# Optimization experiments

Measured on AMD Instinct MI355X. Metric: run time of the kernel, lower is better.

Reference implementation:

```python
import jax, jax.numpy as jnp
import numpy as np

P = 64
K = 64
D = 2048
KERNEL_MUL = 2.0
KERNEL_NUM = 5


def setup_inputs() -> dict:
    key = jax.random.key(0)
    k1, k2 = jax.random.split(key)
    source = jax.random.normal(k1, (P * K, D), dtype=jnp.float32)
    target = jax.random.normal(k2, (P * K, D), dtype=jnp.float32)
    return {"source": source, "target": target}


def _mmd_terms(source, target):
    # split into P groups of K rows each, process all splits at once
    src = source.reshape(P, K, D)
    tgt = target.reshape(P, K, D)
    total = jnp.concatenate([src, tgt], axis=1)          # [P, 2K, D]
    n = 2 * K
    # pairwise squared L2 distances per split: [P, 2K, 2K]
    sq = jnp.sum(total * total, axis=-1)                  # [P, 2K]
    gram = jnp.einsum('pid,pjd->pij', total, total)       # [P, 2K, 2K]
    l2 = sq[:, :, None] + sq[:, None, :] - 2.0 * gram
    # bandwidth from detached distances (torch uses L2_distance.data)
    bw = jax.lax.stop_gradient(jnp.sum(l2, axis=(1, 2))) / (n * n - n)  # [P]
    bw = bw / (KERNEL_MUL ** (KERNEL_NUM // 2))
    mults = KERNEL_MUL ** jnp.arange(KERNEL_NUM, dtype=jnp.float32)     # [kn]
    bws = bw[:, None] * mults[None, :] + 1e-9                           # [P, kn]
    # multi-bandwidth Gaussian kernel sum: [P, 2K, 2K]
    kern = jnp.sum(jnp.exp(-l2[:, None, :, :] / bws[:, :, None, None]), axis=1)
    XX = kern[:, :K, :K]
    YY = kern[:, K:, K:]
    XY = kern[:, :K, K:]
    YX = kern[:, K:, :K]
    xx = jnp.mean(XX, axis=(1, 2))
    yy = jnp.mean(YY, axis=(1, 2))
    xy = jnp.mean(XY, axis=(1, 2))
    yx = jnp.mean(YX, axis=(1, 2))
    per_split_loss = xx + yy - xy - yx                    # [P]
    total_loss = jnp.sum(per_split_loss) / P
    return total_loss, l2, xx, yy, xy, yx


def reference(source, target):
    total_loss, l2, xx, yy, xy, yx = _mmd_terms(source, target)
    # original returns max of l2dist from the LAST split only
    max_l2_last = jnp.max(l2[-1])
    return (total_loss.reshape(1), max_l2_last,
            jnp.sum(xx) / P, jnp.sum(yy) / P, jnp.sum(xy) / P, jnp.sum(yx) / P)
```

## Files before the change

kernel.cpp:

```cpp
#include <hip/hip_runtime.h>

typedef _Float16 half8 __attribute__((ext_vector_type(8)));
typedef _Float16 half4v __attribute__((ext_vector_type(4)));
typedef float floatx4 __attribute__((ext_vector_type(4)));
typedef unsigned int uint2v __attribute__((ext_vector_type(2)));

#define NSPLIT 64
#define KS 64
#define DIM 2048
#define NROW 128
#define BK 128
#define KSPL 4
#define KCH (DIM / KSPL)
#define NKC_A (KCH / BK)
#define SST 152
#define GSZ (NROW * NROW)
#define NBLK (NSPLIT * KSPL)
#define GT2F_OFF (NBLK * GSZ / 2)
#define PART_OFF (GT2F_OFF + NBLK)
#define CNT_OFF (PART_OFF + NBLK * 4)


__device__ __forceinline__ unsigned int pk16(float a, float b) {
  return __builtin_bit_cast(unsigned int, __builtin_amdgcn_cvt_pkrtz(a, b));
}

__global__ __launch_bounds__(1024) void gram_kernel(const float* __restrict__ src,
                                                    const float* __restrict__ tgt,
                                                    float* __restrict__ ws) {
  __shared__ __align__(16) _Float16 stage[2][NROW * SST];
  __shared__ float red[16];

  if (blockIdx.x == 0 && threadIdx.x == 0) *(unsigned*)(ws + CNT_OFF) = 0u;

  const int p = blockIdx.x >> 2;
  const int c = blockIdx.x & (KSPL - 1);
  const int tid = threadIdx.x;
  const int lane = tid & 63;
  const int wave = tid >> 6;

  const int srow = tid >> 3;
  const int c4 = (tid & 7) * 4;
  const float* rowp = ((srow < KS) ? (src + (size_t)(p * KS + srow) * DIM)
                                   : (tgt + (size_t)(p * KS + (srow - KS)) * DIM)) +
                      c * KCH;

  const int wr = (wave >> 2) * 32;
  const int wc = (wave & 3) * 32;
  const int fr = lane & 15;
  const int fk = (lane >> 4) * 8;

  floatx4 acc00 = {0.f, 0.f, 0.f, 0.f};
  floatx4 acc01 = {0.f, 0.f, 0.f, 0.f};
  floatx4 acc10 = {0.f, 0.f, 0.f, 0.f};
  floatx4 acc11 = {0.f, 0.f, 0.f, 0.f};

  float4 f0, f1, f2, f3;
#define LOADK(kc)                                      \
  do {                                                 \
    const float* gp_ = rowp + (kc) * BK + c4;          \
    f0 = *(const float4*)(gp_);                        \
    f1 = *(const float4*)(gp_ + 32);                   \
    f2 = *(const float4*)(gp_ + 64);                   \
    f3 = *(const float4*)(gp_ + 96);                   \
  } while (0)

  LOADK(0);
#pragma unroll
  for (int kc = 0; kc < NKC_A; ++kc) {
    {
      _Float16* sp = &stage[kc & 1][srow * SST + c4];
      *(uint2v*)(sp)      = (uint2v){pk16(f0.x, f0.y), pk16(f0.z, f0.w)};
      *(uint2v*)(sp + 32) = (uint2v){pk16(f1.x, f1.y), pk16(f1.z, f1.w)};
      *(uint2v*)(sp + 64) = (uint2v){pk16(f2.x, f2.y), pk16(f2.z, f2.w)};
      *(uint2v*)(sp + 96) = (uint2v){pk16(f3.x, f3.y), pk16(f3.z, f3.w)};
    }
    if (kc + 1 < NKC_A) LOADK(kc + 1);
    __syncthreads();
    const _Float16* sbuf = stage[kc & 1];
#pragma unroll
    for (int ks = 0; ks < 4; ++ks) {
      const int ko = ks * 32 + fk;
      half8 a0 = *(const half8*)&sbuf[(wr + fr) * SST + ko];
      half8 a1 = *(const half8*)&sbuf[(wr + 16 + fr) * SST + ko];
      half8 b0 = *(const half8*)&sbuf[(wc + fr) * SST + ko];
      half8 b1 = *(const half8*)&sbuf[(wc + 16 + fr) * SST + ko];
      acc00 = __builtin_amdgcn_mfma_f32_16x16x32_f16(a0, b0, acc00, 0, 0, 0);
      acc01 = __builtin_amdgcn_mfma_f32_16x16x32_f16(a0, b1, acc01, 0, 0, 0);
      acc10 = __builtin_amdgcn_mfma_f32_16x16x32_f16(a1, b0, acc10, 0, 0, 0);
      acc11 = __builtin_amdgcn_mfma_f32_16x16x32_f16(a1, b1, acc11, 0, 0, 0);
    }
  }
#undef LOADK

  _Float16* hs = (_Float16*)ws + (size_t)blockIdx.x * GSZ + wave * 1024 + lane * 4;
  {
    half4v h0, h1, h2, h3;
#pragma unroll
    for (int r = 0; r < 4; ++r) {
      h0[r] = (_Float16)acc00[r];
      h1[r] = (_Float16)acc01[r];
      h2[r] = (_Float16)acc10[r];
      h3[r] = (_Float16)acc11[r];
    }
    *(half4v*)(hs)       = h0;
    *(half4v*)(hs + 256) = h1;
    *(half4v*)(hs + 512) = h2;
    *(half4v*)(hs + 768) = h3;
  }

  float gsum = 0.0f;
#pragma unroll
  for (int r = 0; r < 4; ++r) gsum += acc00[r] + acc01[r] + acc10[r] + acc11[r];
#pragma unroll
  for (int m = 1; m <= 32; m <<= 1) gsum += __shfl_xor(gsum, m, 64);
  if (lane == 0) red[wave] = gsum;
  __syncthreads();
  if (tid == 0) {
    float t = 0.0f;
    for (int w = 0; w < 16; ++w) t += red[w];
    ws[GT2F_OFF + blockIdx.x] = t;
  }
}

__global__ __launch_bounds__(1024) void reduce_kernel(float* __restrict__ ws,
                                                      float* __restrict__ out) {
  __shared__ float sqv[NROW];
  __shared__ float bcast[8];
  __shared__ float redm[16];
  __shared__ float redq[16];
  __shared__ float fr2[16][5];
  __shared__ unsigned amLast;

  const int b = blockIdx.x;
  const int p = b >> 2;
  const int rb = b & 3;
  const int tid = threadIdx.x;
  const int lane = tid & 63;
  const int wave = tid >> 6;

  const _Float16* sb = (const _Float16*)ws + (size_t)(p * KSPL) * GSZ;

  const int hoff = rb * 4096 + tid * 4;
  float g0, g1, g2, g3;
  {
    half4v h = *(const half4v*)(sb + hoff);
    g0 = (float)h[0]; g1 = (float)h[1]; g2 = (float)h[2]; g3 = (float)h[3];
#pragma unroll
    for (int c8 = 1; c8 < KSPL; ++c8) {
      half4v hh = *(const half4v*)(sb + (size_t)c8 * GSZ + hoff);
      g0 += (float)hh[0]; g1 += (float)hh[1]; g2 += (float)hh[2]; g3 += (float)hh[3];
    }
  }

  if (tid < NROW) {
    const int i = tid;
    const int wd = (i >> 5) * 5;
    const int ad = ((i >> 4) & 1) * 3;
    const int lnd = (((i & 15) >> 2) << 4) + (i & 15);
    const int idxd = wd * 1024 + ad * 256 + lnd * 4 + (i & 3);
    float d = 0.0f;
#pragma unroll
    for (int c8 = 0; c8 < KSPL; ++c8) d += (float)sb[(size_t)c8 * GSZ + idxd];
    sqv[i] = d;
  }
  __syncthreads();

  if (tid == 0) {
    float ssq = 0.0f;
    for (int i = 0; i < NROW; ++i) ssq += sqv[i];
    float gt = ws[GT2F_OFF + p * 4 + 0] + ws[GT2F_OFF + p * 4 + 1] +
               ws[GT2F_OFF + p * 4 + 2] + ws[GT2F_OFF + p * 4 + 3];
    float suml2 = 2.0f * (float)NROW * ssq - 2.0f * gt;
    float bw = suml2 / (float)(NROW * NROW - NROW) * 0.25f;
    float mult = 1.0f;
    for (int k = 0; k < 5; ++k) {
      bcast[k] = 1.0f / (bw * mult + 1e-9f);
      mult *= 2.0f;
    }
  }
  __syncthreads();

  const int r0 = rb * 32 + ((tid >> 7) & 1) * 16 + ((tid >> 4) & 3) * 4;
  const int col = (tid >> 8) * 32 + ((tid >> 6) & 1) * 16 + (tid & 15);
  const float sqc = sqv[col];
  const floatx4 sr = *(const floatx4*)&sqv[r0];
  const float gg[4] = {g0, g1, g2, g3};
  float l2r[4];
  float lmax = 0.0f;
#pragma unroll
  for (int k = 0; k < 4; ++k) {
    float v = sr[k] + sqc - 2.0f * gg[k];
    l2r[k] = v;
    lmax = fmaxf(lmax, v);
  }
#pragma unroll
  for (int m = 1; m <= 32; m <<= 1) lmax = fmaxf(lmax, __shfl_xor(lmax, m, 64));
  if (lane == 0) redm[wave] = lmax;

  const float ib0 = bcast[0], ib1 = bcast[1], ib2 = bcast[2], ib3 = bcast[3], ib4 = bcast[4];
  float qsum = 0.0f;
#pragma unroll
  for (int k = 0; k < 4; ++k) {
    float v = l2r[k];
    qsum += __expf(-v * ib0) + __expf(-v * ib1) + __expf(-v * ib2) +
            __expf(-v * ib3) + __expf(-v * ib4);
  }
#pragma unroll
  for (int m = 1; m <= 32; m <<= 1) qsum += __shfl_xor(qsum, m, 64);
  if (lane == 0) redq[wave] = qsum;
  __syncthreads();

  if (tid == 0) {
    float qX = 0.0f, qY = 0.0f, mx = 0.0f;
#pragma unroll
    for (int w = 0; w < 8; ++w) qX += redq[w];
#pragma unroll
    for (int w = 8; w < 16; ++w) qY += redq[w];
#pragma unroll
    for (int w = 0; w < 16; ++w) mx = fmaxf(mx, redm[w]);
    float4* part = (float4*)(ws + PART_OFF);
    part[b] = make_float4(qX, qY, mx, 0.0f);
    __threadfence();
    unsigned old = atomicAdd((unsigned*)(ws + CNT_OFF), 1u);
    amLast = (old == NBLK - 1) ? 1u : 0u;
  }
  __syncthreads();

  if (amLast) {
    __threadfence();
    const float4* part = (const float4*)(ws + PART_OFF);
    float xx = 0.f, xy = 0.f, yx = 0.f, yy = 0.f, mx = 0.f;
    if (tid < NBLK) {
      float4 pt = part[tid];
      const int rb2 = tid & 3;
      xx = (rb2 < 2) ? pt.x : 0.0f;
      xy = (rb2 < 2) ? pt.y : 0.0f;
      yx = (rb2 >= 2) ? pt.x : 0.0f;
      yy = (rb2 >= 2) ? pt.y : 0.0f;
      mx = ((tid >> 2) == NSPLIT - 1) ? pt.z : 0.0f;
    }
#pragma unroll
    for (int m = 1; m <= 32; m <<= 1) {
      xx += __shfl_xor(xx, m, 64);
      xy += __shfl_xor(xy, m, 64);
      yx += __shfl_xor(yx, m, 64);
      yy += __shfl_xor(yy, m, 64);
      mx = fmaxf(mx, __shfl_xor(mx, m, 64));
    }
    if (lane == 0) {
      fr2[wave][0] = xx; fr2[wave][1] = xy; fr2[wave][2] = yx; fr2[wave][3] = yy; fr2[wave][4] = mx;
    }
    __syncthreads();
    if (tid == 0) {
      float sxx = 0, sxy = 0, syx = 0, syy = 0, smx = 0;
      for (int w = 0; w < 16; ++w) {
        sxx += fr2[w][0]; sxy += fr2[w][1]; syx += fr2[w][2]; syy += fr2[w][3];
        smx = fmaxf(smx, fr2[w][4]);
      }
      const float inv = 1.0f / (4096.0f * 64.0f);
      out[0] = (sxx + syy - sxy - syx) * inv;
      out[1] = smx;
      out[2] = sxx * inv;
      out[3] = syy * inv;
      out[4] = sxy * inv;
      out[5] = syx * inv;
    }
  }
}

extern "C" void kernel_launch(void* const* d_in, const int* in_sizes, int n_in,
                              void* d_out, int out_size, void* d_ws, size_t ws_size,
                              hipStream_t stream) {
  const float* src = (const float*)d_in[0];
  const float* tgt = (const float*)d_in[1];
  float* out = (float*)d_out;
  float* ws = (float*)d_ws;
  gram_kernel<<<NBLK, 1024, 0, stream>>>(src, tgt, ws);
  reduce_kernel<<<NBLK, 1024, 0, stream>>>(ws, out);
}
```

Measured before the change: 110.5 us.

## Fuse gram and reduce kernels with per-split flag synchronization

Merges the two launches into one kernel. The c==3 block of each split waits on spin flags for its three sibling K-chunk blocks, keeps its own partial gram in LDS instead of global memory, and computes the kernel sums for the whole 128x128 tile. Block remapping interleaves splits so producers and consumers are co-resident, input loads become nontemporal, and the final cross-split reduction waits on a second set of flags. This removes a kernel launch and a global round trip, but relies on all blocks being co-resident to avoid deadlock and puts 64 blocks' worth of exp work on a quarter of the blocks.

```diff
diff --git a/kernel.cpp b/kernel.cpp
--- a/kernel.cpp
+++ b/kernel.cpp
@@ -18,26 +18,38 @@
 #define NBLK (NSPLIT * KSPL)
 #define GT2F_OFF (NBLK * GSZ / 2)
 #define PART_OFF (GT2F_OFF + NBLK)
-#define CNT_OFF (PART_OFF + NBLK * 4)
+#define FLAG_OFF (PART_OFF + 256)
 
 
 __device__ __forceinline__ unsigned int pk16(float a, float b) {
   return __builtin_bit_cast(unsigned int, __builtin_amdgcn_cvt_pkrtz(a, b));
 }
 
-__global__ __launch_bounds__(1024) void gram_kernel(const float* __restrict__ src,
-                                                    const float* __restrict__ tgt,
-                                                    float* __restrict__ ws) {
+__global__ __launch_bounds__(1024) void fused_kernel(const float* __restrict__ src,
+                                                     const float* __restrict__ tgt,
+                                                     float* __restrict__ ws,
+                                                     float* __restrict__ out,
+                                                     unsigned nonce) {
   __shared__ __align__(16) _Float16 stage[2][NROW * SST];
   __shared__ float red[16];
-
-  if (blockIdx.x == 0 && threadIdx.x == 0) *(unsigned*)(ws + CNT_OFF) = 0u;
-
-  const int p = blockIdx.x >> 2;
-  const int c = blockIdx.x & (KSPL - 1);
+  __shared__ float sqv[NROW];
+  __shared__ float bcast[8];
+  __shared__ float redm[16];
+  __shared__ float redqA[16];
+  __shared__ float redqB[16];
+  __shared__ float gsum3;
+  __shared__ unsigned smagic;
+
+  const int b = blockIdx.x;
+  const int p = (b & 7) | ((b >> 5) << 3);
+  const int c = (b >> 3) & 3;
   const int tid = threadIdx.x;
   const int lane = tid & 63;
   const int wave = tid >> 6;
+
+  unsigned* flag1 = (unsigned*)(ws + FLAG_OFF);
+  unsigned* flag2 = flag1 + 192;
+  if (tid == 0) smagic = flag1[256] ^ (2u * nonce + 1u);
 
   const int srow = tid >> 3;
   const int c4 = (tid & 7) * 4;
@@ -55,14 +67,14 @@
   floatx4 acc10 = {0.f, 0.f, 0.f, 0.f};
   floatx4 acc11 = {0.f, 0.f, 0.f, 0.f};
 
-  float4 f0, f1, f2, f3;
-#define LOADK(kc)                                      \
-  do {                                                 \
-    const float* gp_ = rowp + (kc) * BK + c4;          \
-    f0 = *(const float4*)(gp_);                        \
-    f1 = *(const float4*)(gp_ + 32);                   \
-    f2 = *(const float4*)(gp_ + 64);                   \
-    f3 = *(const float4*)(gp_ + 96);                   \
+  floatx4 f0, f1, f2, f3;
+#define LOADK(kc)                                                   \
+  do {                                                              \
+    const floatx4* gp_ = (const floatx4*)(rowp + (kc)*BK + c4);     \
+    f0 = __builtin_nontemporal_load(gp_);                           \
+    f1 = __builtin_nontemporal_load(gp_ + 8);                       \
+    f2 = __builtin_nontemporal_load(gp_ + 16);                      \
+    f3 = __builtin_nontemporal_load(gp_ + 24);                      \
   } while (0)
 
   LOADK(0);
@@ -70,10 +82,10 @@
   for (int kc = 0; kc < NKC_A; ++kc) {
     {
       _Float16* sp = &stage[kc & 1][srow * SST + c4];
-      *(uint2v*)(sp)      = (uint2v){pk16(f0.x, f0.y), pk16(f0.z, f0.w)};
-      *(uint2v*)(sp + 32) = (uint2v){pk16(f1.x, f1.y), pk16(f1.z, f1.w)};
-      *(uint2v*)(sp + 64) = (uint2v){pk16(f2.x, f2.y), pk16(f2.z, f2.w)};
-      *(uint2v*)(sp + 96) = (uint2v){pk16(f3.x, f3.y), pk16(f3.z, f3.w)};
+      *(uint2v*)(sp)      = (uint2v){pk16(f0[0], f0[1]), pk16(f0[2], f0[3])};
+      *(uint2v*)(sp + 32) = (uint2v){pk16(f1[0], f1[1]), pk16(f1[2], f1[3])};
+      *(uint2v*)(sp + 64) = (uint2v){pk16(f2[0], f2[1]), pk16(f2[2], f2[3])};
+      *(uint2v*)(sp + 96) = (uint2v){pk16(f3[0], f3[1]), pk16(f3[2], f3[3])};
     }
     if (kc + 1 < NKC_A) LOADK(kc + 1);
     __syncthreads();
@@ -93,16 +105,16 @@
   }
 #undef LOADK
 
-  _Float16* hs = (_Float16*)ws + (size_t)blockIdx.x * GSZ + wave * 1024 + lane * 4;
-  {
-    half4v h0, h1, h2, h3;
-#pragma unroll
-    for (int r = 0; r < 4; ++r) {
-      h0[r] = (_Float16)acc00[r];
-      h1[r] = (_Float16)acc01[r];
-      h2[r] = (_Float16)acc10[r];
-      h3[r] = (_Float16)acc11[r];
-    }
+  half4v h0, h1, h2, h3;
+#pragma unroll
+  for (int r = 0; r < 4; ++r) {
+    h0[r] = (_Float16)acc00[r];
+    h1[r] = (_Float16)acc01[r];
+    h2[r] = (_Float16)acc10[r];
+    h3[r] = (_Float16)acc11[r];
+  }
+  if (c != 3) {
+    _Float16* hs = (_Float16*)ws + (size_t)(p * KSPL + c) * GSZ + wave * 1024 + lane * 4;
     *(half4v*)(hs)       = h0;
     *(half4v*)(hs + 256) = h1;
     *(half4v*)(hs + 512) = h2;
@@ -116,42 +128,37 @@
   for (int m = 1; m <= 32; m <<= 1) gsum += __shfl_xor(gsum, m, 64);
   if (lane == 0) red[wave] = gsum;
   __syncthreads();
-  if (tid == 0) {
-    float t = 0.0f;
-    for (int w = 0; w < 16; ++w) t += red[w];
-    ws[GT2F_OFF + blockIdx.x] = t;
-  }
-}
-
-__global__ __launch_bounds__(1024) void reduce_kernel(float* __restrict__ ws,
-                                                      float* __restrict__ out) {
-  __shared__ float sqv[NROW];
-  __shared__ float bcast[8];
-  __shared__ float redm[16];
-  __shared__ float redq[16];
-  __shared__ float fr2[16][5];
-  __shared__ unsigned amLast;
-
-  const int b = blockIdx.x;
-  const int p = b >> 2;
-  const int rb = b & 3;
-  const int tid = threadIdx.x;
-  const int lane = tid & 63;
-  const int wave = tid >> 6;
+
+  float tot = 0.0f;
+  if (tid == 0)
+    for (int w = 0; w < 16; ++w) tot += red[w];
+
+  if (c != 3) {
+    if (tid == 0) {
+      ws[GT2F_OFF + p * 4 + c] = tot;
+      __threadfence();
+      atomicExch(&flag1[p * 3 + c], smagic);
+    }
+    return;
+  }
+
+  if (tid == 0) gsum3 = tot;
+  _Float16* lsl = (_Float16*)stage;
+  {
+    _Float16* ls = lsl + wave * 1024 + lane * 4;
+    *(half4v*)(ls)       = h0;
+    *(half4v*)(ls + 256) = h1;
+    *(half4v*)(ls + 512) = h2;
+    *(half4v*)(ls + 768) = h3;
+  }
+  const unsigned mg = smagic;
+  if (tid < 3) {
+    while (atomicAdd(&flag1[p * 3 + tid], 0u) != mg) __builtin_amdgcn_s_sleep(1);
+  }
+  __syncthreads();
+  __threadfence();
 
   const _Float16* sb = (const _Float16*)ws + (size_t)(p * KSPL) * GSZ;
-
-  const int hoff = rb * 4096 + tid * 4;
-  float g0, g1, g2, g3;
-  {
-    half4v h = *(const half4v*)(sb + hoff);
-    g0 = (float)h[0]; g1 = (float)h[1]; g2 = (float)h[2]; g3 = (float)h[3];
-#pragma unroll
-    for (int c8 = 1; c8 < KSPL; ++c8) {
-      half4v hh = *(const half4v*)(sb + (size_t)c8 * GSZ + hoff);
-      g0 += (float)hh[0]; g1 += (float)hh[1]; g2 += (float)hh[2]; g3 += (float)hh[3];
-    }
-  }
 
   if (tid < NROW) {
     const int i = tid;
@@ -161,7 +168,8 @@
     const int idxd = wd * 1024 + ad * 256 + lnd * 4 + (i & 3);
     float d = 0.0f;
 #pragma unroll
-    for (int c8 = 0; c8 < KSPL; ++c8) d += (float)sb[(size_t)c8 * GSZ + idxd];
+    for (int c8 = 0; c8 < 3; ++c8) d += (float)sb[(size_t)c8 * GSZ + idxd];
+    d += (float)lsl[idxd];
     sqv[i] = d;
   }
   __syncthreads();
@@ -170,7 +178,7 @@
     float ssq = 0.0f;
     for (int i = 0; i < NROW; ++i) ssq += sqv[i];
     float gt = ws[GT2F_OFF + p * 4 + 0] + ws[GT2F_OFF + p * 4 + 1] +
-               ws[GT2F_OFF + p * 4 + 2] + ws[GT2F_OFF + p * 4 + 3];
+               ws[GT2F_OFF + p * 4 + 2] + gsum3;
     float suml2 = 2.0f * (float)NROW * ssq - 2.0f * gt;
     float bw = suml2 / (float)(NROW * NROW - NROW) * 0.25f;
     float mult = 1.0f;
@@ -181,90 +189,72 @@
   }
   __syncthreads();
 
-  const int r0 = rb * 32 + ((tid >> 7) & 1) * 16 + ((tid >> 4) & 3) * 4;
+  const float ib0 = bcast[0], ib1 = bcast[1], ib2 = bcast[2], ib3 = bcast[3], ib4 = bcast[4];
+  const int r0b = ((tid >> 7) & 1) * 16 + ((tid >> 4) & 3) * 4;
   const int col = (tid >> 8) * 32 + ((tid >> 6) & 1) * 16 + (tid & 15);
   const float sqc = sqv[col];
-  const floatx4 sr = *(const floatx4*)&sqv[r0];
-  const float gg[4] = {g0, g1, g2, g3};
-  float l2r[4];
-  float lmax = 0.0f;
-#pragma unroll
-  for (int k = 0; k < 4; ++k) {
-    float v = sr[k] + sqc - 2.0f * gg[k];
-    l2r[k] = v;
-    lmax = fmaxf(lmax, v);
-  }
-#pragma unroll
-  for (int m = 1; m <= 32; m <<= 1) lmax = fmaxf(lmax, __shfl_xor(lmax, m, 64));
-  if (lane == 0) redm[wave] = lmax;
-
-  const float ib0 = bcast[0], ib1 = bcast[1], ib2 = bcast[2], ib3 = bcast[3], ib4 = bcast[4];
-  float qsum = 0.0f;
-#pragma unroll
-  for (int k = 0; k < 4; ++k) {
-    float v = l2r[k];
-    qsum += __expf(-v * ib0) + __expf(-v * ib1) + __expf(-v * ib2) +
-            __expf(-v * ib3) + __expf(-v * ib4);
-  }
-#pragma unroll
-  for (int m = 1; m <= 32; m <<= 1) qsum += __shfl_xor(qsum, m, 64);
-  if (lane == 0) redq[wave] = qsum;
+  float sA = 0.0f, sB = 0.0f, lmax = 0.0f;
+#pragma unroll
+  for (int rb2 = 0; rb2 < 4; ++rb2) {
+    const int off = rb2 * 4096 + tid * 4;
+    half4v a0 = *(const half4v*)(sb + off);
+    half4v a1 = *(const half4v*)(sb + GSZ + off);
+    half4v a2 = *(const half4v*)(sb + 2 * (size_t)GSZ + off);
+    half4v a3 = *(const half4v*)(lsl + off);
+    const floatx4 sr = *(const floatx4*)&sqv[rb2 * 32 + r0b];
+    float qsum = 0.0f;
+#pragma unroll
+    for (int k = 0; k < 4; ++k) {
+      float g = (float)a0[k] + (float)a1[k] + (float)a2[k] + (float)a3[k];
+      float v = sr[k] + sqc - 2.0f * g;
+      lmax = fmaxf(lmax, v);
+      qsum += __expf(-v * ib0) + __expf(-v * ib1) + __expf(-v * ib2) +
+              __expf(-v * ib3) + __expf(-v * ib4);
+    }
+    if (rb2 < 2) sA += qsum; else sB += qsum;
+  }
+#pragma unroll
+  for (int m = 1; m <= 32; m <<= 1) {
+    lmax = fmaxf(lmax, __shfl_xor(lmax, m, 64));
+    sA += __shfl_xor(sA, m, 64);
+    sB += __shfl_xor(sB, m, 64);
+  }
+  if (lane == 0) { redm[wave] = lmax; redqA[wave] = sA; redqB[wave] = sB; }
   __syncthreads();
 
   if (tid == 0) {
-    float qX = 0.0f, qY = 0.0f, mx = 0.0f;
-#pragma unroll
-    for (int w = 0; w < 8; ++w) qX += redq[w];
-#pragma unroll
-    for (int w = 8; w < 16; ++w) qY += redq[w];
+    float xx = 0.f, xy = 0.f, yx = 0.f, yy = 0.f, mx = 0.f;
+#pragma unroll
+    for (int w = 0; w < 8; ++w) { xx += redqA[w]; yx += redqB[w]; }
+#pragma unroll
+    for (int w = 8; w < 16; ++w) { xy += redqA[w]; yy += redqB[w]; }
 #pragma unroll
     for (int w = 0; w < 16; ++w) mx = fmaxf(mx, redm[w]);
-    float4* part = (float4*)(ws + PART_OFF);
-    part[b] = make_float4(qX, qY, mx, 0.0f);
+    ((float4*)(ws + PART_OFF))[p] = make_float4(xx, xy, yx, yy);
+    if (p == NSPLIT - 1) out[1] = mx;
     __threadfence();
-    unsigned old = atomicAdd((unsigned*)(ws + CNT_OFF), 1u);
-    amLast = (old == NBLK - 1) ? 1u : 0u;
-  }
-  __syncthreads();
-
-  if (amLast) {
+    atomicExch(&flag2[p], mg);
+  }
+
+  if (p == 0 && tid < 64) {
+    while (atomicAdd(&flag2[tid], 0u) != mg) __builtin_amdgcn_s_sleep(1);
     __threadfence();
-    const float4* part = (const float4*)(ws + PART_OFF);
-    float xx = 0.f, xy = 0.f, yx = 0.f, yy = 0.f, mx = 0.f;
-    if (tid < NBLK) {
-      float4 pt = part[tid];
-      const int rb2 = tid & 3;
-      xx = (rb2 < 2) ? pt.x : 0.0f;
-      xy = (rb2 < 2) ? pt.y : 0.0f;
-      yx = (rb2 >= 2) ? pt.x : 0.0f;
-      yy = (rb2 >= 2) ? pt.y : 0.0f;
-      mx = ((tid >> 2) == NSPLIT - 1) ? pt.z : 0.0f;
-    }
+    float4 pt = ((const float4*)(ws + PART_OFF))[tid];
+    float xx = pt.x, xy = pt.y, yx = pt.z, yy = pt.w;
 #pragma unroll
     for (int m = 1; m <= 32; m <<= 1) {
       xx += __shfl_xor(xx, m, 64);
       xy += __shfl_xor(xy, m, 64);
       yx += __shfl_xor(yx, m, 64);
       yy += __shfl_xor(yy, m, 64);
-      mx = fmaxf(mx, __shfl_xor(mx, m, 64));
-    }
-    if (lane == 0) {
-      fr2[wave][0] = xx; fr2[wave][1] = xy; fr2[wave][2] = yx; fr2[wave][3] = yy; fr2[wave][4] = mx;
-    }
-    __syncthreads();
+    }
     if (tid == 0) {
-      float sxx = 0, sxy = 0, syx = 0, syy = 0, smx = 0;
-      for (int w = 0; w < 16; ++w) {
-        sxx += fr2[w][0]; sxy += fr2[w][1]; syx += fr2[w][2]; syy += fr2[w][3];
-        smx = fmaxf(smx, fr2[w][4]);
-      }
       const float inv = 1.0f / (4096.0f * 64.0f);
-      out[0] = (sxx + syy - sxy - syx) * inv;
-      out[1] = smx;
-      out[2] = sxx * inv;
-      out[3] = syy * inv;
-      out[4] = sxy * inv;
-      out[5] = syx * inv;
+      out[0] = (xx + yy - xy - yx) * inv;
+      out[2] = xx * inv;
+      out[3] = yy * inv;
+      out[4] = xy * inv;
+      out[5] = yx * inv;
     }
   }
 }
@@ -276,6 +266,7 @@
   const float* tgt = (const float*)d_in[1];
   float* out = (float*)d_out;
   float* ws = (float*)d_ws;
-  gram_kernel<<<NBLK, 1024, 0, stream>>>(src, tgt, ws);
-  reduce_kernel<<<NBLK, 1024, 0, stream>>>(ws, out);
+  static unsigned nonce = 0;
+  ++nonce;
+  fused_kernel<<<NBLK, 1024, 0, stream>>>(src, tgt, ws, out, nonce);
 }
```

Result: slower. 127.8 us (+15.7%).
